# Kernel optimization log

Hardware: AMD Instinct MI355X
Metric: run time of the kernel (lower is better)

The kernel has to match this reference:

```python
import math
import jax, jax.numpy as jnp
import numpy as np

EMBED_DIM = 1024
NUM_HEADS = 16
HEAD_DIM = EMBED_DIM // NUM_HEADS
NUM_BUCKETS = 32
MAX_DISTANCE = 128


def _relative_position_bucket(relative_position, num_buckets=NUM_BUCKETS, max_distance=MAX_DISTANCE):
    # Bidirectional T5 bucketing (matches torch reference exactly).
    num_buckets = num_buckets // 2
    relative_buckets = (relative_position > 0).astype(jnp.int32) * num_buckets
    relative_position = jnp.abs(relative_position)
    max_exact = num_buckets // 2
    is_small = relative_position < max_exact
    rp_large = jnp.log(relative_position.astype(jnp.float32) / max_exact) / math.log(max_distance / max_exact)
    rp_large = max_exact + (rp_large * (num_buckets - max_exact)).astype(jnp.int32)
    rp_large = jnp.minimum(rp_large, num_buckets - 1)
    relative_buckets = relative_buckets + jnp.where(is_small, relative_position, rp_large)
    return relative_buckets


def compute_bias(rel_emb, query_length, key_length):
    context_position = jnp.arange(query_length, dtype=jnp.int32)[:, None]
    memory_position = jnp.arange(key_length, dtype=jnp.int32)[None, :]
    relative_position = memory_position - context_position  # [q, k]
    buckets = _relative_position_bucket(relative_position)
    values = rel_emb[buckets]                 # [q, k, h]
    return jnp.transpose(values, (2, 0, 1))[None]  # [1, h, q, k]


def setup_inputs() -> dict:
    key = jax.random.key(0)
    k1, k2, k3, k4 = jax.random.split(key, 4)
    B, S = 2, 2048
    hidden_states = jax.random.normal(k1, (B, S, EMBED_DIM), dtype=jnp.float32)
    scale = 1.0 / math.sqrt(EMBED_DIM)
    W_qkv = jax.random.normal(k2, (EMBED_DIM, 3 * EMBED_DIM), dtype=jnp.float32) * scale
    W_out = jax.random.normal(k3, (EMBED_DIM, EMBED_DIM), dtype=jnp.float32) * scale
    rel_emb = jax.random.normal(k4, (NUM_BUCKETS, NUM_HEADS), dtype=jnp.float32) * 0.02
    return {"hidden_states": hidden_states, "W_qkv": W_qkv, "W_out": W_out, "rel_emb": rel_emb}


def reference(hidden_states, W_qkv, W_out, rel_emb):
    B, S, _ = hidden_states.shape
    qkv = hidden_states @ W_qkv                                # [B, S, 3*D]
    qkv = qkv.reshape(B, S, 3, NUM_HEADS, HEAD_DIM)
    qkv = jnp.transpose(qkv, (0, 3, 2, 1, 4))                  # [B, H, 3, S, dh]
    q, k, v = qkv[:, :, 0], qkv[:, :, 1], qkv[:, :, 2]
    scores = jnp.einsum('bhqd,bhkd->bhqk', q, k)               # no 1/sqrt(d) scaling (T5 style)
    scores = scores + compute_bias(rel_emb, S, S)
    attn = jax.nn.softmax(scores.astype(jnp.float32), axis=-1).astype(scores.dtype)
    out = jnp.einsum('bhqk,bhkd->bhqd', attn, v)               # [B, H, S, dh]
    out = jnp.transpose(out, (0, 2, 1, 3)).reshape(B, S, EMBED_DIM)
    return out @ W_out
```

## Files before the change

### kernel.cpp

```cpp
#include <hip/hip_runtime.h>
#include <hip/hip_bf16.h>
#include <math.h>

typedef _Float16 f16;
typedef __attribute__((ext_vector_type(8))) _Float16 f16x8;
typedef __attribute__((ext_vector_type(4))) _Float16 f16x4;
typedef __attribute__((ext_vector_type(2))) _Float16 f16x2;
typedef __attribute__((ext_vector_type(4))) float f32x4;

#define EMBED 1024
#define NHEADS 16
#define HDIM 64
#define BATCH 2
#define SEQ 2048
#define BS 4096
#define LOG2E 1.4426950408889634f


__device__ __forceinline__ f32x4 mfma16x32(f16x8 a, f16x8 b, f32x4 c) {
  return __builtin_amdgcn_mfma_f32_16x16x32_f16(a, b, c, 0, 0, 0);
}
__device__ __forceinline__ f16x2 cvt_pk(float a, float b) {
  return __builtin_bit_cast(f16x2, __builtin_amdgcn_cvt_pkrtz(a, b));
}
__device__ __forceinline__ void gload_lds16(const f16* __restrict__ g, f16* l) {
  __builtin_amdgcn_global_load_lds(
      (const __attribute__((address_space(1))) void*)g,
      (__attribute__((address_space(3))) void*)l, 16, 0, 0);
}

__global__ void prep_kernel(const float* __restrict__ X, const float* __restrict__ Wqkv,
                            const float* __restrict__ Wout, const float* __restrict__ rel_emb,
                            f16* __restrict__ Xh, f16* __restrict__ Wqkv_t,
                            f16* __restrict__ Wout_t, float* __restrict__ btab) {
  __shared__ float tile[32][33];
  int bid = blockIdx.x, tid = threadIdx.x;
  if (bid < 4096) {
    int i = (bid * 256 + tid) * 4;
    float4 v = *(const float4*)(X + i);
    f16x4 o = { (f16)v.x, (f16)v.y, (f16)v.z, (f16)v.w };
    *(f16x4*)(Xh + i) = o;
  } else if (bid < 8192) {
    const float* in;
    f16* out;
    int N, idx;
    if (bid < 7168) { in = Wqkv; out = Wqkv_t; N = 3072; idx = bid - 4096; }
    else            { in = Wout; out = Wout_t; N = 1024; idx = bid - 7168; }
    int nt = N / 32;
    int n0 = (idx % nt) * 32, k0 = (idx / nt) * 32;
    int tx = tid & 31, ty = tid >> 5;
#pragma unroll
    for (int r = ty; r < 32; r += 8) tile[r][tx] = in[(size_t)(k0 + r) * N + n0 + tx];
    __syncthreads();
#pragma unroll
    for (int r = ty; r < 32; r += 8) out[(size_t)(n0 + r) * 1024 + k0 + tx] = (f16)tile[tx][r];
  } else {
    int idx = (bid - 8192) * 256 + tid;
    if (idx >= 4095) return;
    int rp = idx - 2047;
    int rb = rp > 0 ? 16 : 0;
    int arp = rp < 0 ? -rp : rp;
    int loc;
    if (arp < 8) {
      loc = arp;
    } else {
      float lr = logf((float)arp * 0.125f) * (1.0f / 2.7725887222397811f);
      int t = 8 + (int)(lr * 8.0f);
      loc = t < 15 ? t : 15;
    }
    int bucket = rb + loc;
#pragma unroll
    for (int h = 0; h < 16; h++) btab[h * 4095 + idx] = rel_emb[bucket * 16 + h] * LOG2E;
  }
}

__device__ __forceinline__ void gemm_core(const f16* __restrict__ A, const f16* __restrict__ Bt,
                                          int m0, int n0, int Kdim, f32x4 (&acc)[4][4]) {
  __shared__ __align__(16) f16 As[128 * 32];
  __shared__ __align__(16) f16 Bs[128 * 32];

  int tid = threadIdx.x;
  int lane = tid & 63, wave = tid >> 6;
  int l15 = lane & 15, quad = lane >> 4;
  int wr = (wave >> 1) * 64, wc = (wave & 1) * 64;
  int rowl = lane >> 2;
  int col8 = (lane & 3) * 8;

#pragma unroll
  for (int i = 0; i < 4; i++)
#pragma unroll
    for (int j = 0; j < 4; j++) acc[i][j] = f32x4{0.f, 0.f, 0.f, 0.f};

  for (int kt = 0; kt < Kdim / 32; kt++) {
    int kk = kt * 32;
#pragma unroll
    for (int c = 0; c < 2; c++) {
      int row = wave * 32 + c * 16 + rowl;
      gload_lds16(A + (size_t)(m0 + row) * Kdim + kk + col8, &As[(wave * 32 + c * 16) * 32]);
      gload_lds16(Bt + (size_t)(n0 + row) * Kdim + kk + col8, &Bs[(wave * 32 + c * 16) * 32]);
    }
    __syncthreads();
    f16x8 af[4], bf[4];
#pragma unroll
    for (int i = 0; i < 4; i++) af[i] = *(const f16x8*)(&As[(wr + i * 16 + l15) * 32 + quad * 8]);
#pragma unroll
    for (int j = 0; j < 4; j++) bf[j] = *(const f16x8*)(&Bs[(wc + j * 16 + l15) * 32 + quad * 8]);
#pragma unroll
    for (int i = 0; i < 4; i++)
#pragma unroll
      for (int j = 0; j < 4; j++) acc[i][j] = mfma16x32(af[i], bf[j], acc[i][j]);
    __syncthreads();
  }
}

__global__ __launch_bounds__(256, 3) void gemm_qkv_kernel(
    const f16* __restrict__ Xh, const f16* __restrict__ Wt,
    f16* __restrict__ Q, f16* __restrict__ K_, f16* __restrict__ Vp) {
  f32x4 acc[4][4];
  int m0 = blockIdx.y * 128, n0 = blockIdx.x * 128;
  gemm_core(Xh, Wt, m0, n0, 1024, acc);

  int lane = threadIdx.x & 63, wave = threadIdx.x >> 6;
  int l15 = lane & 15, quad = lane >> 4;
  int wr = (wave >> 1) * 64, wc = (wave & 1) * 64;
  int nq = n0 + wc;
  int which = nq >> 10;
  int h = (nq >> 6) & 15;
  int b = m0 >> 11;

  if (which == 2) {
    int s0 = (m0 & 2047) + wr;
    f16* vbase = Vp + (size_t)(b * 16 + h) * 131072 + (size_t)(s0 >> 6) * 4096;
    int qr_lo = (quad >> 1);
    int joff = (quad & 1) * 4;
#pragma unroll
    for (int i = 0; i < 4; i++) {
      int cc = i >> 1;
      int qr = (i & 1) * 2 + qr_lo;
#pragma unroll
      for (int j = 0; j < 4; j++) {
        f16x4 pk = { (f16)acc[i][j][0], (f16)acc[i][j][1], (f16)acc[i][j][2], (f16)acc[i][j][3] };
        *(f16x4*)(vbase + (cc * 4 + j) * 512 + (qr * 16 + l15) * 8 + joff) = pk;
      }
    }
  } else {
    f16* base = (which == 0) ? Q : K_;
    float sc = (which == 0) ? LOG2E : 1.0f;
#pragma unroll
    for (int i = 0; i < 4; i++) {
#pragma unroll
      for (int j = 0; j < 4; j++) {
        int d = j * 16 + l15;
#pragma unroll
        for (int r = 0; r < 4; r++) {
          int m = m0 + wr + i * 16 + quad * 4 + r;
          int s = m & 2047;
          base[(((size_t)(b * 16 + h) * 2048 + s) << 6) + d] = (f16)(acc[i][j][r] * sc);
        }
      }
    }
  }
}

__global__ void repack_k_kernel(const f16* __restrict__ Kw, f16* __restrict__ Kp) {
  int o = blockIdx.x * 256 + threadIdx.x;
  int lane = o & 63;
  int ct = (o >> 6) & 7;
  int kt = (o >> 9) & 31;
  int bh = o >> 14;
  int c = ct >> 1, t = ct & 1;
  int cc = c >> 1, g = c & 1;
  int l15 = lane & 15, quad = lane >> 4;
  int s = kt * 64 + cc * 32 + ((l15 >> 2) << 3) + (g << 2) + (l15 & 3);
  f16x8 v = *(const f16x8*)(Kw + ((size_t)(bh * 2048 + s) << 6) + t * 32 + quad * 8);
  *(f16x8*)(Kp + (size_t)o * 8) = v;
}

__global__ __launch_bounds__(256, 4) void attn_kernel(
    const f16* __restrict__ Q, const f16* __restrict__ Kp, const f16* __restrict__ Vp,
    const float* __restrict__ btab, f16* __restrict__ O) {
  __shared__ float bias_lds[2112];

  int qt = blockIdx.x, bh = blockIdx.y;
  int qbase = qt * 64;
  int h = bh & 15, b = bh >> 4;
  int tid = threadIdx.x, lane = tid & 63, wave = tid >> 6;
  int l15 = lane & 15, quad = lane >> 4;

  const float* brow = btab + h * 4095 + (1984 - qbase);
  for (int i = tid; i < 2111; i += 256) bias_lds[i] = brow[i];

  const f16* qptr = Q + ((size_t)bh * 2048 + qbase + wave * 16 + l15) * 64 + quad * 8;
  f16x8 qf0 = *(const f16x8*)(qptr);
  f16x8 qf1 = *(const f16x8*)(qptr + 32);

  f32x4 accO[4] = {};
  float m_i = -INFINITY;
  float l_acc = 0.f;

  const f16* kc = Kp + (size_t)bh * 131072 + 1792;
  const f16* vc = Vp + (size_t)bh * 131072 + 1792;
  const int voff = lane * 8;
  const int bofs = quad * 8 - wave * 16 - l15 + 63;

  __syncthreads();

  for (int kt = 0; kt < 32; kt++) {
    const float* bb = &bias_lds[kt * 64 + bofs];
    f32x4 scT[4];
    scT[0] = f32x4{ bb[0],  bb[1],  bb[2],  bb[3]  };
    scT[1] = f32x4{ bb[4],  bb[5],  bb[6],  bb[7]  };
    scT[2] = f32x4{ bb[32], bb[33], bb[34], bb[35] };
    scT[3] = f32x4{ bb[36], bb[37], bb[38], bb[39] };
#pragma unroll
    for (int c = 0; c < 4; c++) {
      f16x8 kf0 = *(const f16x8*)(kc + ((c * 2 + 0) * 512 - 1792) + voff);
      f16x8 kf1 = *(const f16x8*)(kc + ((c * 2 + 1) * 512 - 1792) + voff);
      scT[c] = mfma16x32(kf0, qf0, scT[c]);
      scT[c] = mfma16x32(kf1, qf1, scT[c]);
    }
    f16x8 vf[2][4];
#pragma unroll
    for (int cc = 0; cc < 2; cc++)
#pragma unroll
      for (int dblk = 0; dblk < 4; dblk++)
        vf[cc][dblk] = *(const f16x8*)(vc + ((cc * 4 + dblk) * 512 - 1792) + voff);
    float mp0 = fmaxf(fmaxf(fmaxf(scT[0][0], scT[0][1]), scT[0][2]), scT[0][3]);
    float mp1 = fmaxf(fmaxf(fmaxf(scT[1][0], scT[1][1]), scT[1][2]), scT[1][3]);
    float mp2 = fmaxf(fmaxf(fmaxf(scT[2][0], scT[2][1]), scT[2][2]), scT[2][3]);
    float mp3 = fmaxf(fmaxf(fmaxf(scT[3][0], scT[3][1]), scT[3][2]), scT[3][3]);
    float mp = fmaxf(fmaxf(fmaxf(mp0, mp1), mp2), mp3);
    if (__any(mp > m_i)) {
      float mx = fmaxf(mp, __shfl_xor(mp, 16));
      mx = fmaxf(mx, __shfl_xor(mx, 32));
      float mn = fmaxf(m_i, mx);
      float alpha = __builtin_amdgcn_exp2f(m_i - mn);
      m_i = mn;
      l_acc *= alpha;
      float arow[4];
#pragma unroll
      for (int r = 0; r < 4; r++) arow[r] = __shfl(alpha, quad * 4 + r);
#pragma unroll
      for (int d = 0; d < 4; d++)
#pragma unroll
        for (int r = 0; r < 4; r++) accO[d][r] *= arow[r];
    }
    float mx = m_i;
    f16x4 p[4];
#pragma unroll
    for (int c = 0; c < 4; c++) {
      float e0 = __builtin_amdgcn_exp2f(scT[c][0] - mx);
      float e1 = __builtin_amdgcn_exp2f(scT[c][1] - mx);
      float e2 = __builtin_amdgcn_exp2f(scT[c][2] - mx);
      float e3 = __builtin_amdgcn_exp2f(scT[c][3] - mx);
      l_acc += (e0 + e1) + (e2 + e3);
      f16x2 plo = cvt_pk(e0, e1);
      f16x2 phi = cvt_pk(e2, e3);
      p[c][0] = plo[0]; p[c][1] = plo[1]; p[c][2] = phi[0]; p[c][3] = phi[1];
    }
    f16x8 pp0 = __builtin_shufflevector(p[0], p[1], 0, 1, 2, 3, 4, 5, 6, 7);
    f16x8 pp1 = __builtin_shufflevector(p[2], p[3], 0, 1, 2, 3, 4, 5, 6, 7);
#pragma unroll
    for (int dblk = 0; dblk < 4; dblk++) accO[dblk] = mfma16x32(pp0, vf[0][dblk], accO[dblk]);
#pragma unroll
    for (int dblk = 0; dblk < 4; dblk++) accO[dblk] = mfma16x32(pp1, vf[1][dblk], accO[dblk]);
    kc += 4096;
    vc += 4096;
  }

  float lt = l_acc;
  lt += __shfl_xor(lt, 16);
  lt += __shfl_xor(lt, 32);
  float linv = __builtin_amdgcn_rcpf(lt);
  float lrow[4];
#pragma unroll
  for (int r = 0; r < 4; r++) lrow[r] = __shfl(linv, quad * 4 + r);
#pragma unroll
  for (int dblk = 0; dblk < 4; dblk++) {
#pragma unroll
    for (int r = 0; r < 4; r++) {
      int q = qbase + wave * 16 + quad * 4 + r;
      O[((size_t)(b * 2048 + q) << 10) + h * 64 + dblk * 16 + l15] = (f16)(accO[dblk][r] * lrow[r]);
    }
  }
}

__global__ __launch_bounds__(256, 2) void gemm_out_kernel(
    const f16* __restrict__ Oh, const f16* __restrict__ Wt, float* __restrict__ out) {
  __shared__ __align__(16) f16 As[128 * 32];
  __shared__ __align__(16) f16 Bs[64 * 32];

  int tid = threadIdx.x;
  int lane = tid & 63, wave = tid >> 6;
  int l15 = lane & 15, quad = lane >> 4;
  int rowl = lane >> 2;
  int col8 = (lane & 3) * 8;
  int m0 = blockIdx.y * 128, n0 = blockIdx.x * 64;
  int wr = wave * 32;

  f32x4 acc[2][4];
#pragma unroll
  for (int i = 0; i < 2; i++)
#pragma unroll
    for (int j = 0; j < 4; j++) acc[i][j] = f32x4{0.f, 0.f, 0.f, 0.f};

  for (int kt = 0; kt < 32; kt++) {
    int kk = kt * 32;
#pragma unroll
    for (int c = 0; c < 2; c++) {
      int row = wave * 32 + c * 16 + rowl;
      gload_lds16(Oh + (size_t)(m0 + row) * 1024 + kk + col8, &As[(wave * 32 + c * 16) * 32]);
    }
    {
      int row = wave * 16 + rowl;
      gload_lds16(Wt + (size_t)(n0 + row) * 1024 + kk + col8, &Bs[(wave * 16) * 32]);
    }
    __syncthreads();
    f16x8 af[2], bf[4];
#pragma unroll
    for (int i = 0; i < 2; i++) af[i] = *(const f16x8*)(&As[(wr + i * 16 + l15) * 32 + quad * 8]);
#pragma unroll
    for (int j = 0; j < 4; j++) bf[j] = *(const f16x8*)(&Bs[(j * 16 + l15) * 32 + quad * 8]);
#pragma unroll
    for (int i = 0; i < 2; i++)
#pragma unroll
      for (int j = 0; j < 4; j++) acc[i][j] = mfma16x32(af[i], bf[j], acc[i][j]);
    __syncthreads();
  }

#pragma unroll
  for (int i = 0; i < 2; i++) {
#pragma unroll
    for (int j = 0; j < 4; j++) {
      int n = n0 + j * 16 + l15;
#pragma unroll
      for (int r = 0; r < 4; r++) {
        int m = m0 + wr + i * 16 + quad * 4 + r;
        out[((size_t)m << 10) + n] = acc[i][j][r];
      }
    }
  }
}

extern "C" void kernel_launch(void* const* d_in, const int* in_sizes, int n_in,
                              void* d_out, int out_size, void* d_ws, size_t ws_size,
                              hipStream_t stream) {
  const float* X = (const float*)d_in[0];
  const float* Wqkv = (const float*)d_in[1];
  const float* Wout = (const float*)d_in[2];
  const float* rel = (const float*)d_in[3];

  char* ws = (char*)d_ws;
  f16* Xh     = (f16*)(ws + 0);
  f16* Kp     = (f16*)(ws + 0);
  f16* Wqkv_t = (f16*)(ws + 8388608);
  f16* Wout_t = (f16*)(ws + 14680064);
  f16* Qw     = (f16*)(ws + 16777216);
  f16* Kw     = (f16*)(ws + 25165824);
  f16* Vp     = (f16*)(ws + 33554432);
  f16* Ow     = (f16*)(ws + 41943040);
  float* btab = (float*)(ws + 50331648);

  prep_kernel<<<8208, 256, 0, stream>>>(X, Wqkv, Wout, rel, Xh, Wqkv_t, Wout_t, btab);
  gemm_qkv_kernel<<<dim3(24, 32), 256, 0, stream>>>(Xh, Wqkv_t, Qw, Kw, Vp);
  repack_k_kernel<<<2048, 256, 0, stream>>>(Kw, Kp);
  attn_kernel<<<dim3(32, 32), 256, 0, stream>>>(Qw, Kp, Vp, btab, Ow);
  gemm_out_kernel<<<dim3(16, 32), 256, 0, stream>>>(Ow, Wout_t, (float*)d_out);
}
```

Baseline: 213.8 us.

## Fuse K repack into QKV GEMM epilogue and double-buffer K loads in attention

The QKV GEMM epilogue now writes K directly in the MFMA-fragment packed layout that attention consumes, which removes the separate repack kernel launch and its extra read and write of K. The attention loop is unrolled by two with K fragments for the next tile prefetched into registers while the current tile is processed, and the bias is added after the QK MFMA instead of seeding the accumulator. The direct K epilogue does scattered 2-byte stores, and the prefetch raises register pressure, which may hurt occupancy at the 4-wave launch bound.

```diff
diff --git a/kernel.cpp b/kernel.cpp
--- a/kernel.cpp
+++ b/kernel.cpp
@@ -115,7 +115,7 @@
 
 __global__ __launch_bounds__(256, 3) void gemm_qkv_kernel(
     const f16* __restrict__ Xh, const f16* __restrict__ Wt,
-    f16* __restrict__ Q, f16* __restrict__ K_, f16* __restrict__ Vp) {
+    f16* __restrict__ Q, f16* __restrict__ Kp, f16* __restrict__ Vp) {
   f32x4 acc[4][4];
   int m0 = blockIdx.y * 128, n0 = blockIdx.x * 128;
   gemm_core(Xh, Wt, m0, n0, 1024, acc);
@@ -127,10 +127,10 @@
   int which = nq >> 10;
   int h = (nq >> 6) & 15;
   int b = m0 >> 11;
+  int kt = ((m0 & 2047) + wr) >> 6;
 
   if (which == 2) {
-    int s0 = (m0 & 2047) + wr;
-    f16* vbase = Vp + (size_t)(b * 16 + h) * 131072 + (size_t)(s0 >> 6) * 4096;
+    f16* vbase = Vp + (size_t)(b * 16 + h) * 131072 + (size_t)kt * 4096;
     int qr_lo = (quad >> 1);
     int joff = (quad & 1) * 4;
 #pragma unroll
@@ -143,9 +143,27 @@
         *(f16x4*)(vbase + (cc * 4 + j) * 512 + (qr * 16 + l15) * 8 + joff) = pk;
       }
     }
+  } else if (which == 1) {
+    f16* kbase = Kp + (size_t)(b * 16 + h) * 131072 + (size_t)kt * 4096;
+    int jj = l15 & 7;
+    int qk_half = l15 >> 3;
+    int g = quad & 1;
+    int hi2 = quad >> 1;
+#pragma unroll
+    for (int i = 0; i < 4; i++) {
+      int cc = i >> 1;
+      int m_hi = ((i & 1) * 2 + hi2) * 4;
+#pragma unroll
+      for (int j = 0; j < 4; j++) {
+        int slot = (cc * 2 + g) * 2 + (j >> 1);
+        int quadk = (j & 1) * 2 + qk_half;
+#pragma unroll
+        for (int r = 0; r < 4; r++) {
+          kbase[slot * 512 + (quadk * 16 + m_hi + r) * 8 + jj] = (f16)acc[i][j][r];
+        }
+      }
+    }
   } else {
-    f16* base = (which == 0) ? Q : K_;
-    float sc = (which == 0) ? LOG2E : 1.0f;
 #pragma unroll
     for (int i = 0; i < 4; i++) {
 #pragma unroll
@@ -155,25 +173,11 @@
         for (int r = 0; r < 4; r++) {
           int m = m0 + wr + i * 16 + quad * 4 + r;
           int s = m & 2047;
-          base[(((size_t)(b * 16 + h) * 2048 + s) << 6) + d] = (f16)(acc[i][j][r] * sc);
+          Q[(((size_t)(b * 16 + h) * 2048 + s) << 6) + d] = (f16)(acc[i][j][r] * LOG2E);
         }
       }
     }
   }
-}
-
-__global__ void repack_k_kernel(const f16* __restrict__ Kw, f16* __restrict__ Kp) {
-  int o = blockIdx.x * 256 + threadIdx.x;
-  int lane = o & 63;
-  int ct = (o >> 6) & 7;
-  int kt = (o >> 9) & 31;
-  int bh = o >> 14;
-  int c = ct >> 1, t = ct & 1;
-  int cc = c >> 1, g = c & 1;
-  int l15 = lane & 15, quad = lane >> 4;
-  int s = kt * 64 + cc * 32 + ((l15 >> 2) << 3) + (g << 2) + (l15 & 3);
-  f16x8 v = *(const f16x8*)(Kw + ((size_t)(bh * 2048 + s) << 6) + t * 32 + quad * 8);
-  *(f16x8*)(Kp + (size_t)o * 8) = v;
 }
 
 __global__ __launch_bounds__(256, 4) void attn_kernel(
@@ -198,26 +202,19 @@
   float m_i = -INFINITY;
   float l_acc = 0.f;
 
-  const f16* kc = Kp + (size_t)bh * 131072 + 1792;
-  const f16* vc = Vp + (size_t)bh * 131072 + 1792;
+  const f16* kbase = Kp + (size_t)bh * 131072 + 1792;
+  const f16* vbase = Vp + (size_t)bh * 131072 + 1792;
   const int voff = lane * 8;
   const int bofs = quad * 8 - wave * 16 - l15 + 63;
 
   __syncthreads();
 
-  for (int kt = 0; kt < 32; kt++) {
-    const float* bb = &bias_lds[kt * 64 + bofs];
-    f32x4 scT[4];
-    scT[0] = f32x4{ bb[0],  bb[1],  bb[2],  bb[3]  };
-    scT[1] = f32x4{ bb[4],  bb[5],  bb[6],  bb[7]  };
-    scT[2] = f32x4{ bb[32], bb[33], bb[34], bb[35] };
-    scT[3] = f32x4{ bb[36], bb[37], bb[38], bb[39] };
+  auto do_tile = [&](const f16x8 (&kf)[8], const f16* vc, const float* bb) {
+    f32x4 scT[4] = {};
 #pragma unroll
     for (int c = 0; c < 4; c++) {
-      f16x8 kf0 = *(const f16x8*)(kc + ((c * 2 + 0) * 512 - 1792) + voff);
-      f16x8 kf1 = *(const f16x8*)(kc + ((c * 2 + 1) * 512 - 1792) + voff);
-      scT[c] = mfma16x32(kf0, qf0, scT[c]);
-      scT[c] = mfma16x32(kf1, qf1, scT[c]);
+      scT[c] = mfma16x32(kf[c * 2 + 0], qf0, scT[c]);
+      scT[c] = mfma16x32(kf[c * 2 + 1], qf1, scT[c]);
     }
     f16x8 vf[2][4];
 #pragma unroll
@@ -225,6 +222,10 @@
 #pragma unroll
       for (int dblk = 0; dblk < 4; dblk++)
         vf[cc][dblk] = *(const f16x8*)(vc + ((cc * 4 + dblk) * 512 - 1792) + voff);
+    scT[0] += f32x4{ bb[0],  bb[1],  bb[2],  bb[3]  };
+    scT[1] += f32x4{ bb[4],  bb[5],  bb[6],  bb[7]  };
+    scT[2] += f32x4{ bb[32], bb[33], bb[34], bb[35] };
+    scT[3] += f32x4{ bb[36], bb[37], bb[38], bb[39] };
     float mp0 = fmaxf(fmaxf(fmaxf(scT[0][0], scT[0][1]), scT[0][2]), scT[0][3]);
     float mp1 = fmaxf(fmaxf(fmaxf(scT[1][0], scT[1][1]), scT[1][2]), scT[1][3]);
     float mp2 = fmaxf(fmaxf(fmaxf(scT[2][0], scT[2][1]), scT[2][2]), scT[2][3]);
@@ -264,8 +265,22 @@
     for (int dblk = 0; dblk < 4; dblk++) accO[dblk] = mfma16x32(pp0, vf[0][dblk], accO[dblk]);
 #pragma unroll
     for (int dblk = 0; dblk < 4; dblk++) accO[dblk] = mfma16x32(pp1, vf[1][dblk], accO[dblk]);
-    kc += 4096;
-    vc += 4096;
+  };
+
+  f16x8 k0[8], k1[8];
+#pragma unroll
+  for (int u = 0; u < 8; u++) k0[u] = *(const f16x8*)(kbase + (u * 512 - 1792) + voff);
+
+  for (int ktp = 0; ktp < 16; ktp++) {
+    int ktA = 2 * ktp, ktB = 2 * ktp + 1;
+    const f16* kB = kbase + (size_t)ktB * 4096;
+#pragma unroll
+    for (int u = 0; u < 8; u++) k1[u] = *(const f16x8*)(kB + (u * 512 - 1792) + voff);
+    do_tile(k0, vbase + (size_t)ktA * 4096, &bias_lds[ktA * 64 + bofs]);
+    const f16* kC = kbase + (size_t)(ktB < 31 ? ktB + 1 : ktB) * 4096;
+#pragma unroll
+    for (int u = 0; u < 8; u++) k0[u] = *(const f16x8*)(kC + (u * 512 - 1792) + voff);
+    do_tile(k1, vbase + (size_t)ktB * 4096, &bias_lds[ktB * 64 + bofs]);
   }
 
   float lt = l_acc;
@@ -352,18 +367,16 @@
 
   char* ws = (char*)d_ws;
   f16* Xh     = (f16*)(ws + 0);
-  f16* Kp     = (f16*)(ws + 0);
   f16* Wqkv_t = (f16*)(ws + 8388608);
   f16* Wout_t = (f16*)(ws + 14680064);
   f16* Qw     = (f16*)(ws + 16777216);
-  f16* Kw     = (f16*)(ws + 25165824);
+  f16* Kp     = (f16*)(ws + 25165824);
   f16* Vp     = (f16*)(ws + 33554432);
   f16* Ow     = (f16*)(ws + 41943040);
   float* btab = (float*)(ws + 50331648);
 
   prep_kernel<<<8208, 256, 0, stream>>>(X, Wqkv, Wout, rel, Xh, Wqkv_t, Wout_t, btab);
-  gemm_qkv_kernel<<<dim3(24, 32), 256, 0, stream>>>(Xh, Wqkv_t, Qw, Kw, Vp);
-  repack_k_kernel<<<2048, 256, 0, stream>>>(Kw, Kp);
+  gemm_qkv_kernel<<<dim3(24, 32), 256, 0, stream>>>(Xh, Wqkv_t, Qw, Kp, Vp);
   attn_kernel<<<dim3(32, 32), 256, 0, stream>>>(Qw, Kp, Vp, btab, Ow);
   gemm_out_kernel<<<dim3(16, 32), 256, 0, stream>>>(Ow, Wout_t, (float*)d_out);
 }
```

After: 217.2 us. Within noise of the previous version (+1.6%).
